# Performance work log

Measured on AMD Instinct MI355X. Metric: run time of the kernel, lower is better.

Reference implementation:

```python
import jax, jax.numpy as jnp
import numpy as np

SINGLE_DIM = 256
PAIR_DIM = 64
MAX_REL_POS = 32
LN_EPS = 1e-5


def setup_inputs() -> dict:
    key = jax.random.key(0)
    ks = jax.random.split(key, 6)
    B, N = 2, 1024
    single_repr = jax.random.normal(ks[0], (B, N, SINGLE_DIM), dtype=jnp.float32)
    # Linear(single_dim*2 -> pair_dim)
    lim = 1.0 / np.sqrt(2 * SINGLE_DIM)
    W = jax.random.uniform(ks[1], (2 * SINGLE_DIM, PAIR_DIM), minval=-lim, maxval=lim, dtype=jnp.float32)
    b = jax.random.uniform(ks[2], (PAIR_DIM,), minval=-lim, maxval=lim, dtype=jnp.float32)
    # LayerNorm(pair_dim)
    gamma = jnp.ones((PAIR_DIM,), dtype=jnp.float32)
    beta = jnp.zeros((PAIR_DIM,), dtype=jnp.float32)
    # Embedding(2*max_rel_pos+1, pair_dim)
    embed = jax.random.normal(ks[3], (2 * MAX_REL_POS + 1, PAIR_DIM), dtype=jnp.float32)
    return {"single_repr": single_repr, "W": W, "b": b, "gamma": gamma, "beta": beta, "embed": embed}


def reference(single_repr, W, b, gamma, beta, embed):
    B, N, d = single_repr.shape
    # Split the Linear weight: cat([s_i, s_j]) @ W == s_i @ W_i + s_j @ W_j.
    # This avoids materializing the [B,N,N,2d] concat tensor (outer-sum trick).
    W_i, W_j = W[:d], W[d:]                       # [d, pair_dim] each
    proj_i = jnp.einsum('bnd,dp->bnp', single_repr, W_i)  # [B,N,P]
    proj_j = jnp.einsum('bnd,dp->bnp', single_repr, W_j)  # [B,N,P]
    x = proj_i[:, :, None, :] + proj_j[:, None, :, :] + b  # [B,N,N,P]
    # LayerNorm over last dim
    mu = jnp.mean(x, axis=-1, keepdims=True)
    var = jnp.mean((x - mu) ** 2, axis=-1, keepdims=True)
    x = (x - mu) * jax.lax.rsqrt(var + LN_EPS) * gamma + beta
    x = jax.nn.relu(x)
    # Relative position embedding
    pos = jnp.arange(N)
    rel = jnp.clip(pos[None, :] - pos[:, None], -MAX_REL_POS, MAX_REL_POS) + MAX_REL_POS  # [N,N]
    x = x + embed[rel][None]  # broadcast over batch
    return x
```

## Files before the change

### kernel.cpp

```cpp
#include <hip/hip_runtime.h>

#define SINGLE_DIM 256
#define PAIR_DIM   64
#define MAX_REL    32
#define LN_EPS     1e-5f
#define N_FIXED    1024

typedef float vfloat4 __attribute__((ext_vector_type(4)));

#define DPP_ADD(x, ctrl)                                                    \
    ((x) + __int_as_float(__builtin_amdgcn_update_dpp(                      \
               0, __float_as_int(x), (ctrl), 0xf, 0xf, true)))

__device__ __forceinline__ float rowsum16(float x) {
    x = DPP_ADD(x, 0x128);
    x = DPP_ADD(x, 0x124);
    x = DPP_ADD(x, 0x122);
    x = DPP_ADD(x, 0x121);
    return x;
}

__global__ __launch_bounds__(256) void proj_kernel(
    const float* __restrict__ s,
    const float* __restrict__ W,
    const float* __restrict__ bias,
    float* __restrict__ proj,
    float* __restrict__ rowstats)
{
    __shared__ float lds[2][SINGLE_DIM];
    const int row0 = blockIdx.x * 2;
    const int t = threadIdx.x;

    ((float2*)(&lds[0][0]))[t] = ((const float2*)(s + (size_t)row0 * SINGLE_DIM))[t];
    __syncthreads();

    const int row  = t >> 7;
    const int c    = t & 127;
    const int half = c >> 6;
    const int p    = c & 63;

    const float* wcol = W + half * (SINGLE_DIM * PAIR_DIM) + p;
    const float* srow = lds[row];

    float acc = (half == 0) ? bias[p] : 0.f;
    #pragma unroll 8
    for (int d = 0; d < SINGLE_DIM; ++d)
        acc += srow[d] * wcol[d * PAIR_DIM];

    proj[(size_t)(row0 + row) * 128 + c] = acc;

    if (rowstats) {
        float sv = acc, qv = acc * acc;
        #pragma unroll
        for (int mask = 1; mask < 64; mask <<= 1) {
            sv += __shfl_xor(sv, mask, 64);
            qv += __shfl_xor(qv, mask, 64);
        }
        if ((t & 63) == 0)
            *(float2*)(rowstats + (size_t)(row0 + row) * 4 + half * 2) =
                make_float2(sv, qv);
    }
}

__global__ __launch_bounds__(256, 6) void pair_v3_kernel(
    const float* __restrict__ proj,
    const float* __restrict__ rowstats,
    const float* __restrict__ gamma,
    const float* __restrict__ beta,
    const float* __restrict__ embed,
    float* __restrict__ out)
{
    const int t  = threadIdx.x;
    const int g  = t >> 4;
    const int p0 = (t & 15) * 4;
    const int bid = blockIdx.x;
    const int bi    = bid >> 4;
    const int jbase = (bid & 15) * 64 + g;
    const int i = bi & (N_FIXED - 1);
    const int b = bi >> 10;

    const float4 pi4 = *(const float4*)(proj + (size_t)bi * 128 + p0);
    const float4 g4  = *(const float4*)(gamma + p0);
    const float4 b4  = *(const float4*)(beta + p0);
    const float2 rsi = *(const float2*)(rowstats + (size_t)bi * 4);

    #pragma unroll
    for (int k = 0; k < 4; ++k) {
        const int j = jbase + 16 * k;
        const size_t jrow = (size_t)b * N_FIXED + j;
        const float4 pj4 = *(const float4*)(proj + jrow * 128 + 64 + p0);
        const float2 rsj = *(const float2*)(rowstats + jrow * 4 + 2);

        float4 v;
        v.x = pi4.x + pj4.x;
        v.y = pi4.y + pj4.y;
        v.z = pi4.z + pj4.z;
        v.w = pi4.w + pj4.w;

        float dot = pi4.x * pj4.x + pi4.y * pj4.y + pi4.z * pj4.z + pi4.w * pj4.w;
        dot = rowsum16(dot);

        const float mean = (rsi.x + rsj.x) * (1.f / PAIR_DIM);
        const float ex2  = (rsi.y + rsj.y + 2.f * dot) * (1.f / PAIR_DIM);
        const float rstd = rsqrtf(ex2 - mean * mean + LN_EPS);

        const float Gx = g4.x * rstd, Gy = g4.y * rstd,
                    Gz = g4.z * rstd, Gw = g4.w * rstd;
        const float Bx = fmaf(-mean, Gx, b4.x), By = fmaf(-mean, Gy, b4.y),
                    Bz = fmaf(-mean, Gz, b4.z), Bw = fmaf(-mean, Gw, b4.w);

        int rel = j - i;
        rel = (rel < -MAX_REL) ? -MAX_REL : (rel > MAX_REL ? MAX_REL : rel);
        rel += MAX_REL;
        const float4 e4 = *(const float4*)(embed + rel * PAIR_DIM + p0);

        vfloat4 o;
        o.x = fmaxf(fmaf(v.x, Gx, Bx), 0.f) + e4.x;
        o.y = fmaxf(fmaf(v.y, Gy, By), 0.f) + e4.y;
        o.z = fmaxf(fmaf(v.z, Gz, Bz), 0.f) + e4.z;
        o.w = fmaxf(fmaf(v.w, Gw, Bw), 0.f) + e4.w;

        __builtin_nontemporal_store(o,
            (vfloat4*)(out + ((size_t)bi * N_FIXED + j) * PAIR_DIM + p0));
    }
}

__global__ __launch_bounds__(256) void pair_kernel(
    const float* __restrict__ proj,
    const float* __restrict__ gamma,
    const float* __restrict__ beta,
    const float* __restrict__ embed,
    float* __restrict__ out)
{
    const int t  = threadIdx.x;
    const int g  = t >> 4;
    const int p0 = (t & 15) * 4;
    const int bid = blockIdx.x;
    const int bi    = bid >> 4;
    const int jbase = (bid & 15) * 64 + g;
    const int i = bi & (N_FIXED - 1);
    const int b = bi >> 10;

    const float4 pi4 = *(const float4*)(proj + (size_t)bi * 128 + p0);
    const float4 g4  = *(const float4*)(gamma + p0);
    const float4 b4  = *(const float4*)(beta + p0);

    float4 v[4];
    float  s[4], ss[4];
    #pragma unroll
    for (int k = 0; k < 4; ++k) {
        const int j = jbase + 16 * k;
        const float4 pj4 = *(const float4*)(proj + (size_t)(b * N_FIXED + j) * 128 + 64 + p0);
        v[k].x = pi4.x + pj4.x;
        v[k].y = pi4.y + pj4.y;
        v[k].z = pi4.z + pj4.z;
        v[k].w = pi4.w + pj4.w;
        s[k]  = v[k].x + v[k].y + v[k].z + v[k].w;
        ss[k] = v[k].x * v[k].x + v[k].y * v[k].y + v[k].z * v[k].z + v[k].w * v[k].w;
    }

    #pragma unroll
    for (int mask = 1; mask < 16; mask <<= 1) {
        #pragma unroll
        for (int k = 0; k < 4; ++k) {
            s[k]  += __shfl_xor(s[k],  mask, 64);
            ss[k] += __shfl_xor(ss[k], mask, 64);
        }
    }

    #pragma unroll
    for (int k = 0; k < 4; ++k) {
        const int j = jbase + 16 * k;
        const float mean = s[k] * (1.f / PAIR_DIM);
        const float var  = ss[k] * (1.f / PAIR_DIM) - mean * mean;
        const float rstd = rsqrtf(var + LN_EPS);

        int rel = j - i;
        rel = (rel < -MAX_REL) ? -MAX_REL : (rel > MAX_REL ? MAX_REL : rel);
        rel += MAX_REL;
        const float4 e4 = *(const float4*)(embed + rel * PAIR_DIM + p0);

        vfloat4 o;
        o.x = fmaxf((v[k].x - mean) * rstd * g4.x + b4.x, 0.f) + e4.x;
        o.y = fmaxf((v[k].y - mean) * rstd * g4.y + b4.y, 0.f) + e4.y;
        o.z = fmaxf((v[k].z - mean) * rstd * g4.z + b4.z, 0.f) + e4.z;
        o.w = fmaxf((v[k].w - mean) * rstd * g4.w + b4.w, 0.f) + e4.w;

        __builtin_nontemporal_store(o,
            (vfloat4*)(out + ((size_t)bi * N_FIXED + j) * PAIR_DIM + p0));
    }
}

extern "C" void kernel_launch(void* const* d_in, const int* in_sizes, int n_in,
                              void* d_out, int out_size, void* d_ws, size_t ws_size,
                              hipStream_t stream) {
    const float* s     = (const float*)d_in[0];
    const float* W     = (const float*)d_in[1];
    const float* bias  = (const float*)d_in[2];
    const float* gamma = (const float*)d_in[3];
    const float* beta  = (const float*)d_in[4];
    const float* embed = (const float*)d_in[5];
    float* out  = (float*)d_out;

    const int BN = in_sizes[0] / SINGLE_DIM;

    const size_t sz_proj = (size_t)BN * 128 * sizeof(float);
    const size_t sz_rs   = (size_t)BN * 4 * sizeof(float);
    float* proj     = (float*)d_ws;
    float* rowstats = (float*)((char*)d_ws + sz_proj);

    const int pair_blocks = BN * (N_FIXED / 64);

    if (ws_size >= sz_proj + sz_rs) {
        proj_kernel<<<BN / 2, 256, 0, stream>>>(s, W, bias, proj, rowstats);
        pair_v3_kernel<<<pair_blocks, 256, 0, stream>>>(proj, rowstats, gamma,
                                                        beta, embed, out);
    } else {
        proj_kernel<<<BN / 2, 256, 0, stream>>>(s, W, bias, proj, nullptr);
        pair_kernel<<<pair_blocks, 256, 0, stream>>>(proj, gamma, beta, embed, out);
    }
}
```

Baseline: 529.8 us.

## Tile pair kernel over 8 i-rows per block to reuse j-projections

Each pair block now handles 8 consecutive i rows against a 64-wide j tile. The j projections and row stats are loaded once into registers and reused across all 8 rows. The block index is also remapped so adjacent blocks cover neighbouring j tiles. This cuts repeated proj loads and the block count, at the cost of less parallelism (4096 blocks) and more registers, and it drops the occupancy hint from the launch bounds. The kernel is output-store bound (512 MB written), so the gain is likely limited.

Measured after the change: 553.1 us. 4.4% more time.

```diff
diff --git a/kernel.cpp b/kernel.cpp
--- a/kernel.cpp
+++ b/kernel.cpp
@@ -5,6 +5,7 @@
 #define MAX_REL    32
 #define LN_EPS     1e-5f
 #define N_FIXED    1024
+#define ITILE      8
 
 typedef float vfloat4 __attribute__((ext_vector_type(4)));
 
@@ -62,7 +63,7 @@
     }
 }
 
-__global__ __launch_bounds__(256, 6) void pair_v3_kernel(
+__global__ __launch_bounds__(256) void pair_v4_kernel(
     const float* __restrict__ proj,
     const float* __restrict__ rowstats,
     const float* __restrict__ gamma,
@@ -70,58 +71,72 @@
     const float* __restrict__ embed,
     float* __restrict__ out)
 {
+    const int n  = blockIdx.x;
+    const int x  = n & 7;
+    const int m  = n >> 3;
+    const int jt = x + 8 * (m & 1);
+    const int it = m >> 1;
+
     const int t  = threadIdx.x;
     const int g  = t >> 4;
     const int p0 = (t & 15) * 4;
-    const int bid = blockIdx.x;
-    const int bi    = bid >> 4;
-    const int jbase = (bid & 15) * 64 + g;
-    const int i = bi & (N_FIXED - 1);
-    const int b = bi >> 10;
-
-    const float4 pi4 = *(const float4*)(proj + (size_t)bi * 128 + p0);
-    const float4 g4  = *(const float4*)(gamma + p0);
-    const float4 b4  = *(const float4*)(beta + p0);
-    const float2 rsi = *(const float2*)(rowstats + (size_t)bi * 4);
-
+
+    const int bi0 = it * ITILE;
+    const int b   = bi0 >> 10;
+    const int j0  = jt * 64;
+
+    float4 pj4[4];
+    float2 rsj[4];
     #pragma unroll
     for (int k = 0; k < 4; ++k) {
-        const int j = jbase + 16 * k;
-        const size_t jrow = (size_t)b * N_FIXED + j;
-        const float4 pj4 = *(const float4*)(proj + jrow * 128 + 64 + p0);
-        const float2 rsj = *(const float2*)(rowstats + jrow * 4 + 2);
-
-        float4 v;
-        v.x = pi4.x + pj4.x;
-        v.y = pi4.y + pj4.y;
-        v.z = pi4.z + pj4.z;
-        v.w = pi4.w + pj4.w;
-
-        float dot = pi4.x * pj4.x + pi4.y * pj4.y + pi4.z * pj4.z + pi4.w * pj4.w;
-        dot = rowsum16(dot);
-
-        const float mean = (rsi.x + rsj.x) * (1.f / PAIR_DIM);
-        const float ex2  = (rsi.y + rsj.y + 2.f * dot) * (1.f / PAIR_DIM);
-        const float rstd = rsqrtf(ex2 - mean * mean + LN_EPS);
-
-        const float Gx = g4.x * rstd, Gy = g4.y * rstd,
-                    Gz = g4.z * rstd, Gw = g4.w * rstd;
-        const float Bx = fmaf(-mean, Gx, b4.x), By = fmaf(-mean, Gy, b4.y),
-                    Bz = fmaf(-mean, Gz, b4.z), Bw = fmaf(-mean, Gw, b4.w);
-
-        int rel = j - i;
-        rel = (rel < -MAX_REL) ? -MAX_REL : (rel > MAX_REL ? MAX_REL : rel);
-        rel += MAX_REL;
-        const float4 e4 = *(const float4*)(embed + rel * PAIR_DIM + p0);
-
-        vfloat4 o;
-        o.x = fmaxf(fmaf(v.x, Gx, Bx), 0.f) + e4.x;
-        o.y = fmaxf(fmaf(v.y, Gy, By), 0.f) + e4.y;
-        o.z = fmaxf(fmaf(v.z, Gz, Bz), 0.f) + e4.z;
-        o.w = fmaxf(fmaf(v.w, Gw, Bw), 0.f) + e4.w;
-
-        __builtin_nontemporal_store(o,
-            (vfloat4*)(out + ((size_t)bi * N_FIXED + j) * PAIR_DIM + p0));
+        const size_t jrow = (size_t)b * N_FIXED + j0 + g + 16 * k;
+        pj4[k] = *(const float4*)(proj + jrow * 128 + 64 + p0);
+        rsj[k] = *(const float2*)(rowstats + jrow * 4 + 2);
+    }
+
+    const float4 g4 = *(const float4*)(gamma + p0);
+    const float4 b4 = *(const float4*)(beta + p0);
+
+    #pragma unroll
+    for (int ii = 0; ii < ITILE; ++ii) {
+        const int bi = bi0 + ii;
+        const int i  = bi & (N_FIXED - 1);
+        const float4 pi4 = *(const float4*)(proj + (size_t)bi * 128 + p0);
+        const float2 rsi = *(const float2*)(rowstats + (size_t)bi * 4);
+        const size_t obase = (size_t)bi * N_FIXED;
+
+        #pragma unroll
+        for (int k = 0; k < 4; ++k) {
+            const int j = j0 + g + 16 * k;
+
+            float dot = fmaf(pi4.x, pj4[k].x,
+                        fmaf(pi4.y, pj4[k].y,
+                        fmaf(pi4.z, pj4[k].z, pi4.w * pj4[k].w)));
+            dot = rowsum16(dot);
+
+            const float mean = (rsi.x + rsj[k].x) * (1.f / PAIR_DIM);
+            const float ex2  = (rsi.y + rsj[k].y + 2.f * dot) * (1.f / PAIR_DIM);
+            const float rstd = rsqrtf(ex2 - mean * mean + LN_EPS);
+
+            const float Gx = g4.x * rstd, Gy = g4.y * rstd,
+                        Gz = g4.z * rstd, Gw = g4.w * rstd;
+            const float Bx = fmaf(-mean, Gx, b4.x), By = fmaf(-mean, Gy, b4.y),
+                        Bz = fmaf(-mean, Gz, b4.z), Bw = fmaf(-mean, Gw, b4.w);
+
+            int rel = j - i;
+            rel = (rel < -MAX_REL) ? -MAX_REL : (rel > MAX_REL ? MAX_REL : rel);
+            rel += MAX_REL;
+            const float4 e4 = *(const float4*)(embed + rel * PAIR_DIM + p0);
+
+            vfloat4 o;
+            o.x = fmaxf(fmaf(pi4.x + pj4[k].x, Gx, Bx), 0.f) + e4.x;
+            o.y = fmaxf(fmaf(pi4.y + pj4[k].y, Gy, By), 0.f) + e4.y;
+            o.z = fmaxf(fmaf(pi4.z + pj4[k].z, Gz, Bz), 0.f) + e4.z;
+            o.w = fmaxf(fmaf(pi4.w + pj4[k].w, Gw, Bw), 0.f) + e4.w;
+
+            __builtin_nontemporal_store(o,
+                (vfloat4*)(out + (obase + j) * PAIR_DIM + p0));
+        }
     }
 }
 
@@ -209,14 +224,14 @@
     float* proj     = (float*)d_ws;
     float* rowstats = (float*)((char*)d_ws + sz_proj);
 
-    const int pair_blocks = BN * (N_FIXED / 64);
-
     if (ws_size >= sz_proj + sz_rs) {
         proj_kernel<<<BN / 2, 256, 0, stream>>>(s, W, bias, proj, rowstats);
-        pair_v3_kernel<<<pair_blocks, 256, 0, stream>>>(proj, rowstats, gamma,
-                                                        beta, embed, out);
+        const int blocks = (BN / ITILE) * (N_FIXED / 64);
+        pair_v4_kernel<<<blocks, 256, 0, stream>>>(proj, rowstats, gamma,
+                                                   beta, embed, out);
     } else {
         proj_kernel<<<BN / 2, 256, 0, stream>>>(s, W, bias, proj, nullptr);
-        pair_kernel<<<pair_blocks, 256, 0, stream>>>(proj, gamma, beta, embed, out);
-    }
-}
+        const int blocks = BN * (N_FIXED / 64);
+        pair_kernel<<<blocks, 256, 0, stream>>>(proj, gamma, beta, embed, out);
+    }
+}
```
